# Kernel tuning notes

Hardware: AMD Instinct MI355X
Metric: run time of the kernel (lower is better)

Reference implementation:

```python
import jax, jax.numpy as jnp
import numpy as np

N_NODES = 50000
N_EDGES = 600000
F_DIM = 128


def setup_inputs() -> dict:
    key = jax.random.key(0)
    k_x, k_e, k_w1, k_b1, k_w2, k_b2 = jax.random.split(key, 6)
    x = jax.random.normal(k_x, (N_NODES, F_DIM), dtype=jnp.float32)
    edge_index = jax.random.randint(k_e, (2, N_EDGES), 0, N_NODES, dtype=jnp.int64)
    # nn.Linear-style params (weight is [out, in])
    s1 = 1.0 / np.sqrt(F_DIM)
    w1 = jax.random.uniform(k_w1, (128, F_DIM), jnp.float32, -s1, s1)
    b1 = jax.random.uniform(k_b1, (128,), jnp.float32, -s1, s1)
    s2 = 1.0 / np.sqrt(128)
    w2 = jax.random.uniform(k_w2, (F_DIM, 128), jnp.float32, -s2, s2)
    b2 = jax.random.uniform(k_b2, (F_DIM,), jnp.float32, -s2, s2)
    return {"x": x, "edge_index": edge_index, "w1": w1, "b1": b1, "w2": w2, "b2": b2}


def reference(x, edge_index, w1, b1, w2, b2):
    n = x.shape[0]
    # add_self_loops: append (i, i) for every node
    loops = jnp.arange(n, dtype=edge_index.dtype)
    src = jnp.concatenate([edge_index[0], loops])  # [E + N]
    dst = jnp.concatenate([edge_index[1], loops])  # [E + N]

    def conv(h):
        h = h @ w1.T + b1          # [N, 128]
        h = h @ w2.T + b2          # [N, F]
        msgs = h[src]              # gather source features [E+N, F]
        return jax.ops.segment_sum(msgs, dst, num_segments=n)  # scatter-add

    h = conv(conv(x))
    return jax.nn.log_softmax(h, axis=1)
```

## Files before the change

### kernel.cpp

```cpp
#include <hip/hip_runtime.h>
#include <hip/hip_bf16.h>

#define N_NODES 50000
#define N_EDGES 600000
#define F 128

#define GEMM_BLOCKS 782
#define NBINS 196
#define NHB 64
#define EPB 9375
#define BINCAP 4608

typedef unsigned short bf16_t;
typedef __attribute__((ext_vector_type(8))) short short8v;
typedef __attribute__((ext_vector_type(8))) unsigned short ushort8v;
typedef __attribute__((ext_vector_type(4))) float f32x4;

__device__ inline float bf2f(bf16_t u) {
    union { unsigned int i; float f; } c;
    c.i = ((unsigned int)u) << 16;
    return c.f;
}
__device__ inline bf16_t f2bf(float f) {
    union { float f; unsigned int i; } c;
    c.f = f;
    unsigned int lsb = (c.i >> 16) & 1;
    c.i += 0x7fffu + lsb;
    return (bf16_t)(c.i >> 16);
}

__global__ __launch_bounds__(256)
void k_prep(const float* __restrict__ w1, const float* __restrict__ b1,
            const float* __restrict__ w2, const float* __restrict__ b2,
            float* __restrict__ Wc, float* __restrict__ bc,
            const int* __restrict__ dst, int* __restrict__ cnt2) {
    __shared__ int hist[NBINS];
    int bid = blockIdx.x;
    int tid = threadIdx.x;
    if (bid < 128) {
        int p = bid;
        if (tid < 128) {
            int j = tid;
            float s = 0.f;
            for (int o = 0; o < F; ++o) s = fmaf(w2[p * F + o], w1[o * F + j], s);
            Wc[p * F + j] = s;
            if (j == 0) {
                float t = b2[p];
                for (int o = 0; o < F; ++o) t = fmaf(w2[p * F + o], b1[o], t);
                bc[p] = t;
            }
        }
        return;
    }
    int hb = bid - 128;
    for (int b = tid; b < NBINS; b += 256) hist[b] = 0;
    __syncthreads();
    int e0 = hb * EPB;
    int e1 = min(e0 + EPB, N_EDGES);
    for (int e = e0 + tid; e < e1; e += 256) atomicAdd(&hist[dst[e] >> 8], 1);
    __syncthreads();
    for (int b = tid; b < NBINS; b += 256) cnt2[b * NHB + hb] = hist[b];
}

__global__ __launch_bounds__(1024)
void k_prep2(const float* __restrict__ Wc, const float* __restrict__ bc,
             bf16_t* __restrict__ Mbf, float* __restrict__ v1,
             const int* __restrict__ cnt2, int* __restrict__ wofs2,
             int* __restrict__ binofs) {
    __shared__ int wtot[16];
    int bid = blockIdx.x;
    int t = threadIdx.x;

    if (bid < 16) {
        int kk = bid * 8 + (t >> 7);
        int p = t & 127;
        float s = 0.f;
        for (int o = 0; o < F; ++o) s = fmaf(Wc[p * F + o], Wc[o * F + kk], s);
        Mbf[p * F + kk] = f2bf(s);
        if (bid == 0 && t < 128) {
            float v = 0.f;
            for (int o = 0; o < F; ++o) v = fmaf(Wc[t * F + o], bc[o], v);
            v1[t] = v;
        }
        return;
    }

    const int NV = NBINS * NHB;
    const int CH = 13;
    int lane = t & 63, wv = t >> 6;
    int base = t * CH;
    int s = 0;
    for (int i = 0; i < CH; ++i) {
        int idx = base + i;
        if (idx < NV) s += cnt2[idx];
    }
    int incl = s;
#pragma unroll
    for (int o = 1; o < 64; o <<= 1) {
        int u = __shfl_up(incl, o);
        if (lane >= o) incl += u;
    }
    if (lane == 63) wtot[wv] = incl;
    __syncthreads();
    if (t == 0) {
        int r = 0;
        for (int w = 0; w < 16; ++w) { int x = wtot[w]; wtot[w] = r; r += x; }
    }
    __syncthreads();
    int run = incl - s + wtot[wv];
    for (int i = 0; i < CH; ++i) {
        int idx = base + i;
        if (idx < NV) {
            int w = cnt2[idx];
            wofs2[idx] = run;
            if ((idx & (NHB - 1)) == 0) binofs[idx / NHB] = run;
            run += w;
        }
    }
    if (t == 0) binofs[NBINS] = N_EDGES;
}

__global__ __launch_bounds__(256, 4)
void k_mainB(const float* __restrict__ X, const bf16_t* __restrict__ Mbf,
             bf16_t* __restrict__ G,
             const int* __restrict__ src, const int* __restrict__ dst,
             const int* __restrict__ cnt2, const int* __restrict__ wofs2,
             unsigned int* __restrict__ ebuf) {
    __shared__ __align__(16) unsigned char smem[EPB * 4 + 3 * NBINS * 4 + 16];
    const int bid = blockIdx.x;
    const int tid = threadIdx.x;

    if (bid >= GEMM_BLOCKS) {
        unsigned int* pairs = (unsigned int*)smem;
        int* cur  = (int*)(smem + EPB * 4);
        int* lofs = cur + NBINS;
        int* gofs = lofs + NBINS;
        int* wt4  = gofs + NBINS;
        int hb = bid - GEMM_BLOCKS;

        int c = 0;
        if (tid < NBINS) {
            c = cnt2[tid * NHB + hb];
            gofs[tid] = wofs2[tid * NHB + hb];
        }
        int lane = tid & 63, wv = tid >> 6;
        int incl = c;
#pragma unroll
        for (int o = 1; o < 64; o <<= 1) {
            int u = __shfl_up(incl, o);
            if (lane >= o) incl += u;
        }
        if (lane == 63) wt4[wv] = incl;
        __syncthreads();
        if (tid == 0) {
            int r = 0;
            for (int w = 0; w < 4; ++w) { int x = wt4[w]; wt4[w] = r; r += x; }
        }
        __syncthreads();
        if (tid < NBINS) {
            int e = incl - c + wt4[wv];
            lofs[tid] = e;
            cur[tid] = e;
        }
        __syncthreads();

        int e0 = hb * EPB;
        for (int e = e0 + tid; e < e0 + EPB; e += 256) {
            int d = dst[e];
            int s = src[e];
            unsigned int p = ((unsigned int)d << 16) | (unsigned int)s;
            int slot = atomicAdd(&cur[d >> 8], 1);
            pairs[slot] = p;
        }
        __syncthreads();

        for (int i = tid; i < EPB; i += 256) {
            unsigned int p = pairs[i];
            int b = p >> 24;
            ebuf[gofs[b] + (i - lofs[b])] = p;
        }
        return;
    }

    unsigned short* Xs = (unsigned short*)smem;
    const int row0 = bid * 64;

    for (int idx = tid; idx < 1024; idx += 256) {
        int r = idx >> 4, c = idx & 15;
        int grow = row0 + r;
        float4 va = {0.f, 0.f, 0.f, 0.f}, vb = {0.f, 0.f, 0.f, 0.f};
        if (grow < N_NODES) {
            const float4* xr = (const float4*)(X + (size_t)grow * F);
            va = xr[2 * c];
            vb = xr[2 * c + 1];
        }
        ushort8v u;
        u[0] = f2bf(va.x); u[1] = f2bf(va.y); u[2] = f2bf(va.z); u[3] = f2bf(va.w);
        u[4] = f2bf(vb.x); u[5] = f2bf(vb.y); u[6] = f2bf(vb.z); u[7] = f2bf(vb.w);
        *(ushort8v*)&Xs[r * 128 + (((c ^ (r & 7)) << 3))] = u;
    }
    __syncthreads();

    const int wid = tid >> 6;
    const int lane = tid & 63;
    const int wr = wid >> 1;
    const int wc = wid & 1;
    const int l15 = lane & 15;
    const int l4 = lane >> 4;
    const int sw = (l15 & 7);

    f32x4 acc[2][4] = {};

#pragma unroll
    for (int kc = 0; kc < 4; ++kc) {
        const int cS = ((kc * 4 + l4) ^ sw) << 3;
        short8v a0 = *(const short8v*)&Xs[(wr * 32 + 0 * 16 + l15) * 128 + cS];
        short8v a1 = *(const short8v*)&Xs[(wr * 32 + 1 * 16 + l15) * 128 + cS];
        const bf16_t* mb = Mbf + (size_t)(wc * 64 + l15) * F + kc * 32 + 8 * l4;
        short8v b0 = *(const short8v*)(mb + 0 * 16 * F);
        short8v b1 = *(const short8v*)(mb + 1 * 16 * F);
        short8v b2 = *(const short8v*)(mb + 2 * 16 * F);
        short8v b3 = *(const short8v*)(mb + 3 * 16 * F);
        acc[0][0] = __builtin_amdgcn_mfma_f32_16x16x32_bf16(a0, b0, acc[0][0], 0, 0, 0);
        acc[0][1] = __builtin_amdgcn_mfma_f32_16x16x32_bf16(a0, b1, acc[0][1], 0, 0, 0);
        acc[0][2] = __builtin_amdgcn_mfma_f32_16x16x32_bf16(a0, b2, acc[0][2], 0, 0, 0);
        acc[0][3] = __builtin_amdgcn_mfma_f32_16x16x32_bf16(a0, b3, acc[0][3], 0, 0, 0);
        acc[1][0] = __builtin_amdgcn_mfma_f32_16x16x32_bf16(a1, b0, acc[1][0], 0, 0, 0);
        acc[1][1] = __builtin_amdgcn_mfma_f32_16x16x32_bf16(a1, b1, acc[1][1], 0, 0, 0);
        acc[1][2] = __builtin_amdgcn_mfma_f32_16x16x32_bf16(a1, b2, acc[1][2], 0, 0, 0);
        acc[1][3] = __builtin_amdgcn_mfma_f32_16x16x32_bf16(a1, b3, acc[1][3], 0, 0, 0);
    }

#pragma unroll
    for (int mt = 0; mt < 2; ++mt) {
#pragma unroll
        for (int nt = 0; nt < 4; ++nt) {
#pragma unroll
            for (int r = 0; r < 4; ++r) {
                int grow = row0 + wr * 32 + mt * 16 + l4 * 4 + r;
                if (grow < N_NODES) {
                    int gcol = wc * 64 + nt * 16 + l15;
                    G[(size_t)grow * F + gcol] = f2bf(acc[mt][nt][r]);
                }
            }
        }
    }
}

__global__ __launch_bounds__(1024)
void k_fineagg(const unsigned int* __restrict__ ebuf, const int* __restrict__ binofs,
               const bf16_t* __restrict__ g,
               int* __restrict__ cnt, int* __restrict__ rofs,
               unsigned short* __restrict__ csr, bf16_t* __restrict__ a1) {
    __shared__ unsigned int pairs[BINCAP];
    __shared__ unsigned short ssrc[BINCAP];
    __shared__ int hcnt[256];
    __shared__ int hofs[256];
    __shared__ int cur[256];
    __shared__ int wtot[4];
    const int b = blockIdx.x;
    const int t = threadIdx.x;
    const int r0 = binofs[b];
    const int m = binofs[b + 1] - r0;

    for (int i = t; i < m; i += 1024) pairs[i] = ebuf[r0 + i];
    if (t < 256) hcnt[t] = 0;
    __syncthreads();
    for (int i = t; i < m; i += 1024) atomicAdd(&hcnt[(pairs[i] >> 16) & 255], 1);
    __syncthreads();

    int v = 0, incl = 0;
    int lane = t & 63, wv = t >> 6;
    if (t < 256) {
        v = hcnt[t];
        incl = v;
#pragma unroll
        for (int o = 1; o < 64; o <<= 1) {
            int u = __shfl_up(incl, o);
            if (lane >= o) incl += u;
        }
        if (lane == 63) wtot[wv] = incl;
    }
    __syncthreads();
    if (t == 0) {
        int r = 0;
        for (int w = 0; w < 4; ++w) { int x = wtot[w]; wtot[w] = r; r += x; }
    }
    __syncthreads();
    if (t < 256) {
        int excl = incl - v + wtot[wv];
        hofs[t] = excl;
        cur[t] = excl;
        int node = b * 256 + t;
        if (node < N_NODES) { cnt[node] = v; rofs[node] = r0 + excl; }
        else if (node == N_NODES) rofs[node] = N_EDGES;
    }
    __syncthreads();

    for (int i = t; i < m; i += 1024) {
        unsigned int u = pairs[i];
        int d8 = (u >> 16) & 255;
        int slot = atomicAdd(&cur[d8], 1);
        ssrc[slot] = (unsigned short)(u & 0xFFFF);
    }
    __syncthreads();
    for (int i = t; i < m; i += 1024) csr[r0 + i] = ssrc[i];

    const int lane16 = t & 15;
    const int grp = t >> 4;
    for (int ln = grp; ln < 256; ln += 64) {
        int node = b * 256 + ln;
        if (node >= N_NODES) continue;
        int deg = hcnt[ln];
        int rl = hofs[ln];

        ushort8v u = ((const ushort8v*)(g + (size_t)node * F))[lane16];
        float a0 = bf2f(u[0]), a1_ = bf2f(u[1]), a2 = bf2f(u[2]), a3 = bf2f(u[3]);
        float a4 = bf2f(u[4]), a5 = bf2f(u[5]), a6 = bf2f(u[6]), a7 = bf2f(u[7]);

        int i = 0;
        for (; i + 4 <= deg; i += 4) {
            int s0 = ssrc[rl + i], s1 = ssrc[rl + i + 1];
            int s2 = ssrc[rl + i + 2], s3 = ssrc[rl + i + 3];
            ushort8v u0 = ((const ushort8v*)(g + (size_t)s0 * F))[lane16];
            ushort8v u1 = ((const ushort8v*)(g + (size_t)s1 * F))[lane16];
            ushort8v u2 = ((const ushort8v*)(g + (size_t)s2 * F))[lane16];
            ushort8v u3 = ((const ushort8v*)(g + (size_t)s3 * F))[lane16];
            a0 += bf2f(u0[0]) + bf2f(u1[0]) + bf2f(u2[0]) + bf2f(u3[0]);
            a1_ += bf2f(u0[1]) + bf2f(u1[1]) + bf2f(u2[1]) + bf2f(u3[1]);
            a2 += bf2f(u0[2]) + bf2f(u1[2]) + bf2f(u2[2]) + bf2f(u3[2]);
            a3 += bf2f(u0[3]) + bf2f(u1[3]) + bf2f(u2[3]) + bf2f(u3[3]);
            a4 += bf2f(u0[4]) + bf2f(u1[4]) + bf2f(u2[4]) + bf2f(u3[4]);
            a5 += bf2f(u0[5]) + bf2f(u1[5]) + bf2f(u2[5]) + bf2f(u3[5]);
            a6 += bf2f(u0[6]) + bf2f(u1[6]) + bf2f(u2[6]) + bf2f(u3[6]);
            a7 += bf2f(u0[7]) + bf2f(u1[7]) + bf2f(u2[7]) + bf2f(u3[7]);
        }
        for (; i < deg; ++i) {
            int s = ssrc[rl + i];
            ushort8v uv = ((const ushort8v*)(g + (size_t)s * F))[lane16];
            a0 += bf2f(uv[0]); a1_ += bf2f(uv[1]); a2 += bf2f(uv[2]); a3 += bf2f(uv[3]);
            a4 += bf2f(uv[4]); a5 += bf2f(uv[5]); a6 += bf2f(uv[6]); a7 += bf2f(uv[7]);
        }
        ushort8v o;
        o[0] = f2bf(a0); o[1] = f2bf(a1_); o[2] = f2bf(a2); o[3] = f2bf(a3);
        o[4] = f2bf(a4); o[5] = f2bf(a5); o[6] = f2bf(a6); o[7] = f2bf(a7);
        ((ushort8v*)(a1 + (size_t)node * F))[lane16] = o;
    }
}

__global__ __launch_bounds__(256)
void k_agg_ep(const bf16_t* __restrict__ H, const int* __restrict__ rofs,
              const unsigned short* __restrict__ csr, const int* __restrict__ cnt,
              const float* __restrict__ v1, const float* __restrict__ bc,
              float* __restrict__ O, int n_rows) {
    int tid = threadIdx.x;
    int lane = tid & 15;
    int node = blockIdx.x * 16 + (tid >> 4);
    if (node >= n_rows) return;

    int r0 = rofs[node];
    int deg = rofs[node + 1] - r0;

    ushort8v u = ((const ushort8v*)(H + (size_t)node * F))[lane];
    float a0 = bf2f(u[0]), a1 = bf2f(u[1]), a2 = bf2f(u[2]), a3 = bf2f(u[3]);
    float a4 = bf2f(u[4]), a5 = bf2f(u[5]), a6 = bf2f(u[6]), a7 = bf2f(u[7]);

    const unsigned short* bk = csr + r0;

    int sdi = (lane == 0) ? (deg + 1) : 0;
    for (int j = lane; j < deg; j += 16) sdi += cnt[bk[j]] + 1;

    int i = 0;
    for (; i + 4 <= deg; i += 4) {
        int s0 = bk[i + 0], s1 = bk[i + 1], s2 = bk[i + 2], s3 = bk[i + 3];
        ushort8v u0 = ((const ushort8v*)(H + (size_t)s0 * F))[lane];
        ushort8v u1 = ((const ushort8v*)(H + (size_t)s1 * F))[lane];
        ushort8v u2 = ((const ushort8v*)(H + (size_t)s2 * F))[lane];
        ushort8v u3 = ((const ushort8v*)(H + (size_t)s3 * F))[lane];
        a0 += bf2f(u0[0]) + bf2f(u1[0]) + bf2f(u2[0]) + bf2f(u3[0]);
        a1 += bf2f(u0[1]) + bf2f(u1[1]) + bf2f(u2[1]) + bf2f(u3[1]);
        a2 += bf2f(u0[2]) + bf2f(u1[2]) + bf2f(u2[2]) + bf2f(u3[2]);
        a3 += bf2f(u0[3]) + bf2f(u1[3]) + bf2f(u2[3]) + bf2f(u3[3]);
        a4 += bf2f(u0[4]) + bf2f(u1[4]) + bf2f(u2[4]) + bf2f(u3[4]);
        a5 += bf2f(u0[5]) + bf2f(u1[5]) + bf2f(u2[5]) + bf2f(u3[5]);
        a6 += bf2f(u0[6]) + bf2f(u1[6]) + bf2f(u2[6]) + bf2f(u3[6]);
        a7 += bf2f(u0[7]) + bf2f(u1[7]) + bf2f(u2[7]) + bf2f(u3[7]);
    }
    for (; i < deg; ++i) {
        ushort8v uv = ((const ushort8v*)(H + (size_t)bk[i] * F))[lane];
        a0 += bf2f(uv[0]); a1 += bf2f(uv[1]); a2 += bf2f(uv[2]); a3 += bf2f(uv[3]);
        a4 += bf2f(uv[4]); a5 += bf2f(uv[5]); a6 += bf2f(uv[6]); a7 += bf2f(uv[7]);
    }

#pragma unroll
    for (int o = 8; o; o >>= 1) sdi += __shfl_xor(sdi, o);
    float sdn = (float)sdi;
    float dn = (float)(deg + 1);
    float4 v1a = ((const float4*)v1)[2 * lane], v1b = ((const float4*)v1)[2 * lane + 1];
    float4 bca = ((const float4*)bc)[2 * lane], bcb = ((const float4*)bc)[2 * lane + 1];
    a0 += sdn * v1a.x + dn * bca.x;
    a1 += sdn * v1a.y + dn * bca.y;
    a2 += sdn * v1a.z + dn * bca.z;
    a3 += sdn * v1a.w + dn * bca.w;
    a4 += sdn * v1b.x + dn * bcb.x;
    a5 += sdn * v1b.y + dn * bcb.y;
    a6 += sdn * v1b.z + dn * bcb.z;
    a7 += sdn * v1b.w + dn * bcb.w;

    float m = fmaxf(fmaxf(fmaxf(a0, a1), fmaxf(a2, a3)),
                    fmaxf(fmaxf(a4, a5), fmaxf(a6, a7)));
#pragma unroll
    for (int o = 8; o; o >>= 1) m = fmaxf(m, __shfl_xor(m, o));
    float s = expf(a0 - m) + expf(a1 - m) + expf(a2 - m) + expf(a3 - m)
            + expf(a4 - m) + expf(a5 - m) + expf(a6 - m) + expf(a7 - m);
#pragma unroll
    for (int o = 8; o; o >>= 1) s += __shfl_xor(s, o);
    float lse = m + logf(s);
    float4 oa, ob;
    oa.x = a0 - lse; oa.y = a1 - lse; oa.z = a2 - lse; oa.w = a3 - lse;
    ob.x = a4 - lse; ob.y = a5 - lse; ob.z = a6 - lse; ob.w = a7 - lse;
    ((float4*)(O + (size_t)node * F))[2 * lane] = oa;
    ((float4*)(O + (size_t)node * F))[2 * lane + 1] = ob;
}

extern "C" void kernel_launch(void* const* d_in, const int* in_sizes, int n_in,
                              void* d_out, int out_size, void* d_ws, size_t ws_size,
                              hipStream_t stream) {
    const float* x  = (const float*)d_in[0];
    const int* ei   = (const int*)d_in[1];
    const float* w1 = (const float*)d_in[2];
    const float* b1 = (const float*)d_in[3];
    const float* w2 = (const float*)d_in[4];
    const float* b2 = (const float*)d_in[5];
    float* out = (float*)d_out;

    const int* src = ei;
    const int* dst = ei + N_EDGES;

    float* ws        = (float*)d_ws;
    float* Wc        = ws;
    float* bc        = ws + 16384;
    float* v1        = ws + 16512;
    bf16_t* Mbf      = (bf16_t*)(ws + 16640);
    int*   cnt       = (int*)(ws + 24832);
    int*   rofs      = (int*)(ws + 74880);
    int*   cnt2      = (int*)(ws + 124928);
    int*   wofs2     = (int*)(ws + 137728);
    int*   binofs    = (int*)(ws + 150528);
    unsigned int* ebuf = (unsigned int*)(ws + 150784);
    unsigned short* csr = (unsigned short*)(ws + 750784);
    bf16_t* g        = (bf16_t*)(ws + 1050784);
    bf16_t* a1       = (bf16_t*)(ws + 4250784);

    const int node_grid = (N_NODES + 15) / 16;

    k_prep<<<128 + NHB, 256, 0, stream>>>(w1, b1, w2, b2, Wc, bc, dst, cnt2);
    k_prep2<<<17, 1024, 0, stream>>>(Wc, bc, Mbf, v1, cnt2, wofs2, binofs);
    k_mainB<<<GEMM_BLOCKS + NHB, 256, 0, stream>>>(x, Mbf, g, src, dst,
                                                   cnt2, wofs2, ebuf);
    k_fineagg<<<NBINS, 1024, 0, stream>>>(ebuf, binofs, g, cnt, rofs, csr, a1);
    k_agg_ep<<<node_grid, 256, 0, stream>>>(a1, rofs, csr, cnt, v1, bc, out, N_NODES);
}
```

Baseline: 116.3 us.

## Merge prep kernels, recompute bin offsets per consumer, sort CSR sources

Folds the two prep kernels into one launch. A single 1024-thread block computes the combined weight in shared memory and then the squared matrix M and the bias terms, while the other blocks build per-chunk destination histograms. The global prefix-scan kernel is removed: k_mainB and k_fineagg each recompute the offsets they need directly from cnt2. k_fineagg also insertion-sorts each node's source list so later gathers touch memory in order. The goal is fewer launches and dependency steps, at the cost of serialising the two 128x128 matmuls in one block and adding redundant scan work.

```diff
diff --git a/kernel.cpp b/kernel.cpp
--- a/kernel.cpp
+++ b/kernel.cpp
@@ -29,103 +29,60 @@
     return (bf16_t)(c.i >> 16);
 }
 
-__global__ __launch_bounds__(256)
+__global__ __launch_bounds__(1024)
 void k_prep(const float* __restrict__ w1, const float* __restrict__ b1,
             const float* __restrict__ w2, const float* __restrict__ b2,
-            float* __restrict__ Wc, float* __restrict__ bc,
+            bf16_t* __restrict__ Mbf, float* __restrict__ v1g,
+            float* __restrict__ bcg,
             const int* __restrict__ dst, int* __restrict__ cnt2) {
-    __shared__ int hist[NBINS];
-    int bid = blockIdx.x;
-    int tid = threadIdx.x;
-    if (bid < 128) {
-        int p = bid;
-        if (tid < 128) {
-            int j = tid;
-            float s = 0.f;
-            for (int o = 0; o < F; ++o) s = fmaf(w2[p * F + o], w1[o * F + j], s);
-            Wc[p * F + j] = s;
-            if (j == 0) {
-                float t = b2[p];
-                for (int o = 0; o < F; ++o) t = fmaf(w2[p * F + o], b1[o], t);
-                bc[p] = t;
-            }
-        }
-        return;
-    }
-    int hb = bid - 128;
-    for (int b = tid; b < NBINS; b += 256) hist[b] = 0;
-    __syncthreads();
-    int e0 = hb * EPB;
-    int e1 = min(e0 + EPB, N_EDGES);
-    for (int e = e0 + tid; e < e1; e += 256) atomicAdd(&hist[dst[e] >> 8], 1);
-    __syncthreads();
-    for (int b = tid; b < NBINS; b += 256) cnt2[b * NHB + hb] = hist[b];
-}
-
-__global__ __launch_bounds__(1024)
-void k_prep2(const float* __restrict__ Wc, const float* __restrict__ bc,
-             bf16_t* __restrict__ Mbf, float* __restrict__ v1,
-             const int* __restrict__ cnt2, int* __restrict__ wofs2,
-             int* __restrict__ binofs) {
-    __shared__ int wtot[16];
     int bid = blockIdx.x;
     int t = threadIdx.x;
 
-    if (bid < 16) {
-        int kk = bid * 8 + (t >> 7);
-        int p = t & 127;
-        float s = 0.f;
-        for (int o = 0; o < F; ++o) s = fmaf(Wc[p * F + o], Wc[o * F + kk], s);
-        Mbf[p * F + kk] = f2bf(s);
-        if (bid == 0 && t < 128) {
-            float v = 0.f;
-            for (int o = 0; o < F; ++o) v = fmaf(Wc[t * F + o], bc[o], v);
-            v1[t] = v;
+    if (bid == 0) {
+        __shared__ float WcS[128 * 128];
+        __shared__ float bcS[128];
+        for (int idx = t; idx < 16384; idx += 1024) {
+            int p = idx >> 7, j = idx & 127;
+            float s = 0.f;
+            for (int o = 0; o < 128; ++o) s = fmaf(w2[p * 128 + o], w1[o * 128 + j], s);
+            WcS[idx] = s;
+        }
+        if (t < 128) {
+            float s = b2[t];
+            for (int o = 0; o < 128; ++o) s = fmaf(w2[t * 128 + o], b1[o], s);
+            bcS[t] = s;
+            bcg[t] = s;
+        }
+        __syncthreads();
+        for (int idx = t; idx < 16384; idx += 1024) {
+            int p = idx >> 7, k = idx & 127;
+            float s = 0.f;
+            for (int o = 0; o < 128; ++o) s = fmaf(WcS[p * 128 + o], WcS[o * 128 + k], s);
+            Mbf[idx] = f2bf(s);
+        }
+        if (t < 128) {
+            float s = 0.f;
+            for (int o = 0; o < 128; ++o) s = fmaf(WcS[t * 128 + o], bcS[o], s);
+            v1g[t] = s;
         }
         return;
     }
 
-    const int NV = NBINS * NHB;
-    const int CH = 13;
-    int lane = t & 63, wv = t >> 6;
-    int base = t * CH;
-    int s = 0;
-    for (int i = 0; i < CH; ++i) {
-        int idx = base + i;
-        if (idx < NV) s += cnt2[idx];
-    }
-    int incl = s;
-#pragma unroll
-    for (int o = 1; o < 64; o <<= 1) {
-        int u = __shfl_up(incl, o);
-        if (lane >= o) incl += u;
-    }
-    if (lane == 63) wtot[wv] = incl;
-    __syncthreads();
-    if (t == 0) {
-        int r = 0;
-        for (int w = 0; w < 16; ++w) { int x = wtot[w]; wtot[w] = r; r += x; }
-    }
-    __syncthreads();
-    int run = incl - s + wtot[wv];
-    for (int i = 0; i < CH; ++i) {
-        int idx = base + i;
-        if (idx < NV) {
-            int w = cnt2[idx];
-            wofs2[idx] = run;
-            if ((idx & (NHB - 1)) == 0) binofs[idx / NHB] = run;
-            run += w;
-        }
-    }
-    if (t == 0) binofs[NBINS] = N_EDGES;
+    __shared__ int hist[NBINS];
+    int hb = bid - 1;
+    for (int b = t; b < NBINS; b += 1024) hist[b] = 0;
+    __syncthreads();
+    int e0 = hb * EPB;
+    for (int e = e0 + t; e < e0 + EPB; e += 1024) atomicAdd(&hist[dst[e] >> 8], 1);
+    __syncthreads();
+    for (int b = t; b < NBINS; b += 1024) cnt2[b * NHB + hb] = hist[b];
 }
 
 __global__ __launch_bounds__(256, 4)
 void k_mainB(const float* __restrict__ X, const bf16_t* __restrict__ Mbf,
              bf16_t* __restrict__ G,
              const int* __restrict__ src, const int* __restrict__ dst,
-             const int* __restrict__ cnt2, const int* __restrict__ wofs2,
-             unsigned int* __restrict__ ebuf) {
+             const int* __restrict__ cnt2, unsigned int* __restrict__ ebuf) {
     __shared__ __align__(16) unsigned char smem[EPB * 4 + 3 * NBINS * 4 + 16];
     const int bid = blockIdx.x;
     const int tid = threadIdx.x;
@@ -137,14 +94,24 @@
         int* gofs = lofs + NBINS;
         int* wt4  = gofs + NBINS;
         int hb = bid - GEMM_BLOCKS;
-
-        int c = 0;
+        int lane = tid & 63, wv = tid >> 6;
+
+        int c = 0, colpre = 0, btot = 0;
         if (tid < NBINS) {
+            const int4* row = (const int4*)(cnt2 + tid * NHB);
+            for (int h4 = 0; h4 < NHB / 4; ++h4) {
+                int4 w = row[h4];
+                btot += w.x + w.y + w.z + w.w;
+                int base = h4 * 4;
+                if (base + 0 < hb) colpre += w.x;
+                if (base + 1 < hb) colpre += w.y;
+                if (base + 2 < hb) colpre += w.z;
+                if (base + 3 < hb) colpre += w.w;
+            }
             c = cnt2[tid * NHB + hb];
-            gofs[tid] = wofs2[tid * NHB + hb];
-        }
-        int lane = tid & 63, wv = tid >> 6;
-        int incl = c;
+        }
+
+        int incl = btot;
 #pragma unroll
         for (int o = 1; o < 64; o <<= 1) {
             int u = __shfl_up(incl, o);
@@ -157,8 +124,24 @@
             for (int w = 0; w < 4; ++w) { int x = wt4[w]; wt4[w] = r; r += x; }
         }
         __syncthreads();
+        if (tid < NBINS) gofs[tid] = incl - btot + wt4[wv] + colpre;
+        __syncthreads();
+
+        int incl2 = c;
+#pragma unroll
+        for (int o = 1; o < 64; o <<= 1) {
+            int u = __shfl_up(incl2, o);
+            if (lane >= o) incl2 += u;
+        }
+        if (lane == 63) wt4[wv] = incl2;
+        __syncthreads();
+        if (tid == 0) {
+            int r = 0;
+            for (int w = 0; w < 4; ++w) { int x = wt4[w]; wt4[w] = r; r += x; }
+        }
+        __syncthreads();
         if (tid < NBINS) {
-            int e = incl - c + wt4[wv];
+            int e = incl2 - c + wt4[wv];
             lofs[tid] = e;
             cur[tid] = e;
         }
@@ -248,7 +231,7 @@
 }
 
 __global__ __launch_bounds__(1024)
-void k_fineagg(const unsigned int* __restrict__ ebuf, const int* __restrict__ binofs,
+void k_fineagg(const unsigned int* __restrict__ ebuf, const int* __restrict__ cnt2,
                const bf16_t* __restrict__ g,
                int* __restrict__ cnt, int* __restrict__ rofs,
                unsigned short* __restrict__ csr, bf16_t* __restrict__ a1) {
@@ -257,11 +240,34 @@
     __shared__ int hcnt[256];
     __shared__ int hofs[256];
     __shared__ int cur[256];
-    __shared__ int wtot[4];
+    __shared__ int wtot[16];
+    __shared__ int r0s, ms;
     const int b = blockIdx.x;
     const int t = threadIdx.x;
-    const int r0 = binofs[b];
-    const int m = binofs[b + 1] - r0;
+    const int lane = t & 63, wv = t >> 6;
+
+    const int lim = b * NHB;
+    int part = 0;
+    for (int idx = t; idx < lim; idx += 1024) part += cnt2[idx];
+#pragma unroll
+    for (int o = 32; o; o >>= 1) part += __shfl_xor(part, o);
+    if (lane == 0) wtot[wv] = part;
+    int mv = 0;
+    if (t < 64) {
+        mv = cnt2[lim + t];
+#pragma unroll
+        for (int o = 32; o; o >>= 1) mv += __shfl_xor(mv, o);
+    }
+    __syncthreads();
+    if (t == 0) {
+        int r = 0;
+        for (int w = 0; w < 16; ++w) r += wtot[w];
+        r0s = r;
+        ms = mv;
+    }
+    __syncthreads();
+    const int r0 = r0s;
+    const int m = ms;
 
     for (int i = t; i < m; i += 1024) pairs[i] = ebuf[r0 + i];
     if (t < 256) hcnt[t] = 0;
@@ -270,7 +276,6 @@
     __syncthreads();
 
     int v = 0, incl = 0;
-    int lane = t & 63, wv = t >> 6;
     if (t < 256) {
         v = hcnt[t];
         incl = v;
@@ -302,6 +307,20 @@
         int d8 = (u >> 16) & 255;
         int slot = atomicAdd(&cur[d8], 1);
         ssrc[slot] = (unsigned short)(u & 0xFFFF);
+    }
+    __syncthreads();
+
+    if (t < 256) {
+        int beg = hofs[t], n = hcnt[t];
+        for (int i = 1; i < n; ++i) {
+            unsigned short key = ssrc[beg + i];
+            int j = i - 1;
+            while (j >= 0 && ssrc[beg + j] > key) {
+                ssrc[beg + j + 1] = ssrc[beg + j];
+                --j;
+            }
+            ssrc[beg + j + 1] = key;
+        }
     }
     __syncthreads();
     for (int i = t; i < m; i += 1024) csr[r0 + i] = ssrc[i];
@@ -438,26 +457,21 @@
     const int* dst = ei + N_EDGES;
 
     float* ws        = (float*)d_ws;
-    float* Wc        = ws;
-    float* bc        = ws + 16384;
-    float* v1        = ws + 16512;
-    bf16_t* Mbf      = (bf16_t*)(ws + 16640);
-    int*   cnt       = (int*)(ws + 24832);
-    int*   rofs      = (int*)(ws + 74880);
-    int*   cnt2      = (int*)(ws + 124928);
-    int*   wofs2     = (int*)(ws + 137728);
-    int*   binofs    = (int*)(ws + 150528);
-    unsigned int* ebuf = (unsigned int*)(ws + 150784);
-    unsigned short* csr = (unsigned short*)(ws + 750784);
-    bf16_t* g        = (bf16_t*)(ws + 1050784);
-    bf16_t* a1       = (bf16_t*)(ws + 4250784);
+    float* bc        = ws;
+    float* v1        = ws + 128;
+    bf16_t* Mbf      = (bf16_t*)(ws + 256);
+    int*   cnt       = (int*)(ws + 8448);
+    int*   rofs      = (int*)(ws + 58496);
+    int*   cnt2      = (int*)(ws + 108544);
+    unsigned int* ebuf = (unsigned int*)(ws + 121344);
+    unsigned short* csr = (unsigned short*)(ws + 721344);
+    bf16_t* g        = (bf16_t*)(ws + 1021344);
+    bf16_t* a1       = (bf16_t*)(ws + 4221344);
 
     const int node_grid = (N_NODES + 15) / 16;
 
-    k_prep<<<128 + NHB, 256, 0, stream>>>(w1, b1, w2, b2, Wc, bc, dst, cnt2);
-    k_prep2<<<17, 1024, 0, stream>>>(Wc, bc, Mbf, v1, cnt2, wofs2, binofs);
-    k_mainB<<<GEMM_BLOCKS + NHB, 256, 0, stream>>>(x, Mbf, g, src, dst,
-                                                   cnt2, wofs2, ebuf);
-    k_fineagg<<<NBINS, 1024, 0, stream>>>(ebuf, binofs, g, cnt, rofs, csr, a1);
+    k_prep<<<1 + NHB, 1024, 0, stream>>>(w1, b1, w2, b2, Mbf, v1, bc, dst, cnt2);
+    k_mainB<<<GEMM_BLOCKS + NHB, 256, 0, stream>>>(x, Mbf, g, src, dst, cnt2, ebuf);
+    k_fineagg<<<NBINS, 1024, 0, stream>>>(ebuf, cnt2, g, cnt, rofs, csr, a1);
     k_agg_ep<<<node_grid, 256, 0, stream>>>(a1, rofs, csr, cnt, v1, bc, out, N_NODES);
 }
```

Result: slower. 391.8 us (+237.0%).
